# Kernel tuning notes

Measured on AMD Instinct MI355X. Metric: run time of the kernel, lower is better.

Reference implementation:

```python
import jax, jax.numpy as jnp
import numpy as np

N_FEAT = 7          # input_vector_size
M = 3               # memberships per feature (hardcoded 3 in torch module)
FUZZ = M ** N_FEAT  # 2187, cartesian product size
MID = 512
NUM_CLASS = 10
BATCH = 4096

# Precompute cartesian-product index table: itertools.product over rows of u[i]
# (last feature index varies fastest). IDX[k, i] = which of the 3 memberships of
# feature i appears in combination k.
_k = np.arange(FUZZ)
IDX = ((_k[:, None] // (M ** np.arange(N_FEAT - 1, -1, -1))[None, :]) % M).astype(np.int32)  # [FUZZ, N_FEAT]


def setup_inputs() -> dict:
    key = jax.random.key(0)
    ks = jax.random.split(key, 8)
    x = jax.random.normal(ks[0], (BATCH, N_FEAT), dtype=jnp.float32)
    # Parameters (xavier-ish init for weights, ones for b/bais as in torch init)
    c = jax.random.uniform(ks[1], (N_FEAT, M), minval=-1.0, maxval=1.0, dtype=jnp.float32)
    b = jnp.ones((N_FEAT, M), dtype=jnp.float32)
    wei = jax.random.uniform(ks[2], (FUZZ * N_FEAT, FUZZ), minval=-0.01, maxval=0.01, dtype=jnp.float32)
    bais = jnp.ones((1,), dtype=jnp.float32)
    W1 = jax.random.normal(ks[3], (MID, FUZZ), dtype=jnp.float32) * (1.0 / np.sqrt(FUZZ))
    b1 = jnp.zeros((MID,), dtype=jnp.float32)
    W2 = jax.random.normal(ks[4], (FUZZ, MID), dtype=jnp.float32) * (1.0 / np.sqrt(MID))
    b2 = jnp.zeros((FUZZ,), dtype=jnp.float32)
    W3 = jax.random.normal(ks[5], (NUM_CLASS, FUZZ), dtype=jnp.float32) * (1.0 / np.sqrt(FUZZ))
    b3 = jnp.zeros((NUM_CLASS,), dtype=jnp.float32)
    return {"x": x, "c": c, "b": b, "wei": wei, "bais": bais,
            "W1": W1, "b1": b1, "W2": W2, "b2": b2, "W3": W3, "b3": b3}


def reference(x, c, b, wei, bais, W1, b1, W2, b2, W3, b3):
    B = x.shape[0]
    # Gaussian fuzzy memberships: u[b, i, j] = exp(-(x[b,i]-c[i,j])^2 / b[i,j]^2)
    u = jnp.exp(-((x[:, :, None] - c[None]) ** 2) / (b[None] ** 2))  # [B, N_FEAT, M]
    # Cartesian product: dd[bt, k, i] = u[bt, i, IDX[k, i]]  (replaces itertools.product)
    idx = jnp.asarray(IDX)                       # [FUZZ, N_FEAT]
    feat = jnp.arange(N_FEAT)[None, :]           # [1, N_FEAT] broadcasts to [FUZZ, N_FEAT]
    dd = u[:, feat, idx]                         # [B, FUZZ, N_FEAT]
    # Fuzzy rule layer
    a = dd.reshape(B, FUZZ * N_FEAT) @ wei + bais            # [B, FUZZ]
    a_mean = a / jnp.sum(a, axis=1, keepdims=True)
    # Small residual MLP
    h1 = a_mean @ W1.T + b1                                   # [B, MID]
    h2 = h1 @ W2.T + b2                                       # [B, FUZZ]
    h3 = (a_mean + h2) @ W3.T + b3                            # [B, NUM_CLASS]
    out = jax.nn.leaky_relu(h3, negative_slope=0.2)
    # Dropout(0.5) omitted (eval mode / deterministic baseline)
    return out
```

## Files before the change

kernel.cpp:

```cpp
#include <hip/hip_runtime.h>

#define FUZZ 2187
#define NFEAT 7
#define MID 512
#define NCLS 10
#define BATCH 4096
#define SSTR 2192
#define NCH 243
#define PROWS 11
#define PSTR 2188
#define NF4 546

__device__ __forceinline__ void f4add(float4& a, const float4& b) {
    a.x += b.x; a.y += b.y; a.z += b.z; a.w += b.w;
}

__global__ __launch_bounds__(192) void k_reduce_wei(const float* __restrict__ wei,
                                                    float* __restrict__ Spart) {
    int n4 = blockIdx.x * 192 + threadIdx.x;
    if (n4 > NF4) return;
    int by = blockIdx.y;
    const float* base = wei + (size_t)(by * 9) * 7 * FUZZ;
    float* outp = Spart + (size_t)by * PROWS * PSTR;

    if (n4 < NF4) {
        float4 acc[PROWS];
#pragma unroll
        for (int r = 0; r < PROWS; ++r) acc[r] = make_float4(0.f, 0.f, 0.f, 0.f);
#pragma unroll
        for (int kk = 0; kk < 9; ++kk) {
            const float* rp = base + (size_t)kk * 7 * FUZZ + 4 * n4;
            float4 v0 = *(const float4*)(rp);
            float4 v1 = *(const float4*)(rp + (size_t)1 * FUZZ);
            float4 v2 = *(const float4*)(rp + (size_t)2 * FUZZ);
            float4 v3 = *(const float4*)(rp + (size_t)3 * FUZZ);
            float4 v4 = *(const float4*)(rp + (size_t)4 * FUZZ);
            float4 v5 = *(const float4*)(rp + (size_t)5 * FUZZ);
            float4 v6 = *(const float4*)(rp + (size_t)6 * FUZZ);
            f4add(acc[0], v0);
            f4add(acc[1], v1);
            f4add(acc[2], v2);
            f4add(acc[3], v3);
            f4add(acc[4], v4);
            f4add(acc[5 + kk / 3], v5);
            f4add(acc[8 + kk % 3], v6);
        }
#pragma unroll
        for (int r = 0; r < PROWS; ++r)
            *(float4*)(outp + (size_t)r * PSTR + 4 * n4) = acc[r];
    } else {
        float acc[PROWS][3];
#pragma unroll
        for (int r = 0; r < PROWS; ++r)
            for (int c = 0; c < 3; ++c) acc[r][c] = 0.f;
#pragma unroll
        for (int kk = 0; kk < 9; ++kk) {
            const float* rp = base + (size_t)kk * 7 * FUZZ + 2184;
#pragma unroll
            for (int j = 0; j < 7; ++j) {
                int row = (j < 5) ? j : ((j == 5) ? 5 + kk / 3 : 8 + kk % 3);
#pragma unroll
                for (int c = 0; c < 3; ++c)
                    acc[row][c] += rp[(size_t)j * FUZZ + c];
            }
        }
#pragma unroll
        for (int r = 0; r < PROWS; ++r)
            for (int c = 0; c < 3; ++c)
                outp[(size_t)r * PSTR + 2184 + c] = acc[r][c];
    }
}

__global__ __launch_bounds__(192) void k_reduce2(const float* __restrict__ Spart,
                                                 float* __restrict__ S) {
    int n4 = blockIdx.x * 192 + threadIdx.x;
    if (n4 > NF4) return;
    int t = blockIdx.y;
    int j = t / 3, m = t % 3;

    if (n4 < NF4) {
        float4 s = make_float4(0.f, 0.f, 0.f, 0.f);
        if (j < 5) {
            const int place[5] = {81, 27, 9, 3, 1};
            int ops[4];
            int o = 0;
            for (int q = 0; q < 5; ++q)
                if (q != j) ops[o++] = place[q];
            int byb = m * place[j];
            for (int c = 0; c < 81; ++c) {
                int by = byb + (c / 27) * ops[0] + ((c / 9) % 3) * ops[1]
                             + ((c / 3) % 3) * ops[2] + (c % 3) * ops[3];
                f4add(s, *(const float4*)(Spart + ((size_t)by * PROWS + j) * PSTR + 4 * n4));
            }
        } else {
            int row = (j == 5) ? 5 + m : 8 + m;
            for (int by = 0; by < NCH; ++by)
                f4add(s, *(const float4*)(Spart + ((size_t)by * PROWS + row) * PSTR + 4 * n4));
        }
        *(float4*)(S + (size_t)t * SSTR + 4 * n4) = s;
    } else {
        float s0 = 0.f, s1 = 0.f, s2 = 0.f;
        if (j < 5) {
            const int place[5] = {81, 27, 9, 3, 1};
            int ops[4];
            int o = 0;
            for (int q = 0; q < 5; ++q)
                if (q != j) ops[o++] = place[q];
            int byb = m * place[j];
            for (int c = 0; c < 81; ++c) {
                int by = byb + (c / 27) * ops[0] + ((c / 9) % 3) * ops[1]
                             + ((c / 3) % 3) * ops[2] + (c % 3) * ops[3];
                const float* p = Spart + ((size_t)by * PROWS + j) * PSTR + 2184;
                s0 += p[0]; s1 += p[1]; s2 += p[2];
            }
        } else {
            int row = (j == 5) ? 5 + m : 8 + m;
            for (int by = 0; by < NCH; ++by) {
                const float* p = Spart + ((size_t)by * PROWS + row) * PSTR + 2184;
                s0 += p[0]; s1 += p[1]; s2 += p[2];
            }
        }
        S[(size_t)t * SSTR + 2184] = s0;
        S[(size_t)t * SSTR + 2185] = s1;
        S[(size_t)t * SSTR + 2186] = s2;
    }
}

__device__ __forceinline__ float wave_sum(float v) {
#pragma unroll
    for (int off = 32; off > 0; off >>= 1) v += __shfl_down(v, off, 64);
    return v;
}

__global__ __launch_bounds__(256) void k_sw1(const float* __restrict__ S,
                                             const float* __restrict__ W1,
                                             float* __restrict__ SW1,
                                             float* __restrict__ ws1) {
    int i = blockIdx.x;
    int tid = threadIdx.x;
    float acc[21];
    float aw = 0.f;
#pragma unroll
    for (int t = 0; t < 21; ++t) acc[t] = 0.f;
    for (int n = tid; n < FUZZ; n += 256) {
        float w1 = W1[(size_t)i * FUZZ + n];
        aw += w1;
#pragma unroll
        for (int t = 0; t < 21; ++t) acc[t] += S[t * SSTR + n] * w1;
    }
#pragma unroll
    for (int t = 0; t < 21; ++t) acc[t] = wave_sum(acc[t]);
    aw = wave_sum(aw);
    __shared__ float red[4][22];
    int w = tid >> 6, lane = tid & 63;
    if (lane == 0) {
#pragma unroll
        for (int t = 0; t < 21; ++t) red[w][t] = acc[t];
        red[w][21] = aw;
    }
    __syncthreads();
    if (tid < 22) {
        float v = red[0][tid] + red[1][tid] + red[2][tid] + red[3][tid];
        if (tid < 21) SW1[tid * MID + i] = v;
        else          ws1[i] = v;
    }
}

__global__ __launch_bounds__(64) void k_g(const float* __restrict__ SW1,
                                          const float* __restrict__ ws1,
                                          const float* __restrict__ b1,
                                          const float* __restrict__ W2,
                                          float* __restrict__ G,
                                          float* __restrict__ q,
                                          float* __restrict__ p) {
    int n = blockIdx.x;
    int lane = threadIdx.x;
    float acc[21];
    float aq = 0.f, ap = 0.f;
#pragma unroll
    for (int t = 0; t < 21; ++t) acc[t] = 0.f;
    for (int i = lane; i < MID; i += 64) {
        float w2 = W2[(size_t)n * MID + i];
        aq += ws1[i] * w2;
        ap += b1[i] * w2;
#pragma unroll
        for (int t = 0; t < 21; ++t) acc[t] += SW1[t * MID + i] * w2;
    }
#pragma unroll
    for (int t = 0; t < 21; ++t) acc[t] = wave_sum(acc[t]);
    aq = wave_sum(aq);
    ap = wave_sum(ap);
    if (lane == 0) {
#pragma unroll
        for (int t = 0; t < 21; ++t) G[t * SSTR + n] = acc[t];
        q[n] = aq;
        p[n] = ap;
    }
}

__global__ __launch_bounds__(1024) void k_h(const float* __restrict__ S,
                                            const float* __restrict__ G,
                                            const float* __restrict__ q,
                                            const float* __restrict__ p,
                                            const float* __restrict__ b2,
                                            const float* __restrict__ b3,
                                            const float* __restrict__ W3,
                                            float* __restrict__ H,
                                            float* __restrict__ v,
                                            float* __restrict__ w,
                                            float* __restrict__ T) {
    int c = blockIdx.x;
    int tid = threadIdx.x;
    int wv = tid >> 6, lane = tid & 63;
    __shared__ float red[16][24];
    float acc[21];
#pragma unroll
    for (int t = 0; t < 21; ++t) acc[t] = 0.f;
    if (c < NCLS) {
        float av = 0.f, aw = 0.f;
        for (int n = tid; n < FUZZ; n += 1024) {
            float w3 = W3[(size_t)c * FUZZ + n];
            av += (1.0f + q[n]) * w3;
            aw += (p[n] + b2[n]) * w3;
#pragma unroll
            for (int t = 0; t < 21; ++t)
                acc[t] += (S[t * SSTR + n] + G[t * SSTR + n]) * w3;
        }
#pragma unroll
        for (int t = 0; t < 21; ++t) acc[t] = wave_sum(acc[t]);
        av = wave_sum(av);
        aw = wave_sum(aw);
        if (lane == 0) {
#pragma unroll
            for (int t = 0; t < 21; ++t) red[wv][t] = acc[t];
            red[wv][21] = av;
            red[wv][22] = aw;
        }
        __syncthreads();
        if (tid < 23) {
            float s = 0.f;
#pragma unroll
            for (int k = 0; k < 16; ++k) s += red[k][tid];
            if (tid < 21)       H[tid * NCLS + c] = s;
            else if (tid == 21) v[c] = s;
            else                w[c] = s + b3[c];
        }
    } else {
        for (int n = tid; n < FUZZ; n += 1024) {
#pragma unroll
            for (int t = 0; t < 21; ++t) acc[t] += S[t * SSTR + n];
        }
#pragma unroll
        for (int t = 0; t < 21; ++t) acc[t] = wave_sum(acc[t]);
        if (lane == 0) {
#pragma unroll
            for (int t = 0; t < 21; ++t) red[wv][t] = acc[t];
        }
        __syncthreads();
        if (tid < 21) {
            float s = 0.f;
#pragma unroll
            for (int k = 0; k < 16; ++k) s += red[k][tid];
            T[tid] = s;
        }
    }
}

__global__ __launch_bounds__(256) void k_out(const float* __restrict__ x,
                                             const float* __restrict__ cc,
                                             const float* __restrict__ bbv,
                                             const float* __restrict__ bais,
                                             const float* __restrict__ T,
                                             const float* __restrict__ H,
                                             const float* __restrict__ v,
                                             const float* __restrict__ w,
                                             float* __restrict__ out) {
    int b = blockIdx.x * 256 + threadIdx.x;
    if (b >= BATCH) return;
    float xv[NFEAT];
#pragma unroll
    for (int j = 0; j < NFEAT; ++j) xv[j] = x[b * NFEAT + j];
    float u[21];
#pragma unroll
    for (int j = 0; j < NFEAT; ++j) {
#pragma unroll
        for (int m = 0; m < 3; ++m) {
            float d = xv[j] - cc[j * 3 + m];
            float bv = bbv[j * 3 + m];
            u[j * 3 + m] = expf(-(d * d) / (bv * bv));
        }
    }
    float ba = bais[0];
    float r = 2187.0f * ba;
#pragma unroll
    for (int t = 0; t < 21; ++t) r += u[t] * T[t];
    float inv = 1.0f / r;
#pragma unroll
    for (int c = 0; c < NCLS; ++c) {
        float s = 0.f;
#pragma unroll
        for (int t = 0; t < 21; ++t) s += u[t] * H[t * NCLS + c];
        float h = (s + ba * v[c]) * inv + w[c];
        out[b * NCLS + c] = (h >= 0.f) ? h : 0.2f * h;
    }
}

extern "C" void kernel_launch(void* const* d_in, const int* in_sizes, int n_in,
                              void* d_out, int out_size, void* d_ws, size_t ws_size,
                              hipStream_t stream) {
    const float* x    = (const float*)d_in[0];
    const float* c    = (const float*)d_in[1];
    const float* bbv  = (const float*)d_in[2];
    const float* wei  = (const float*)d_in[3];
    const float* bais = (const float*)d_in[4];
    const float* W1   = (const float*)d_in[5];
    const float* b1   = (const float*)d_in[6];
    const float* W2   = (const float*)d_in[7];
    const float* b2   = (const float*)d_in[8];
    const float* W3   = (const float*)d_in[9];
    const float* b3   = (const float*)d_in[10];

    float* ws    = (float*)d_ws;
    float* Spart = ws;
    float* S     = Spart + 5848528;
    float* G     = S + 21 * SSTR;
    float* SW1   = G + 21 * SSTR;
    float* ws1   = SW1 + 21 * MID;
    float* q     = ws1 + MID;
    float* p     = q + SSTR;
    float* T     = p + SSTR;
    float* H     = T + 32;
    float* v     = H + 224;
    float* w     = v + 16;

    k_reduce_wei<<<dim3(3, NCH), 192, 0, stream>>>(wei, Spart);
    k_reduce2<<<dim3(3, 21), 192, 0, stream>>>(Spart, S);
    k_sw1<<<MID, 256, 0, stream>>>(S, W1, SW1, ws1);
    k_g<<<FUZZ, 64, 0, stream>>>(SW1, ws1, b1, W2, G, q, p);
    k_h<<<NCLS + 1, 1024, 0, stream>>>(S, G, q, p, b2, b3, W3, H, v, w, T);
    k_out<<<(BATCH + 255) / 256, 256, 0, stream>>>(x, c, bbv, bais, T, H, v, w,
                                                   (float*)d_out);
}
```

Measured before the change: 305.1 us.

## Split wei reduction across row groups and vectorize reduction kernels with float4

Adds a z grid dimension to the wei reduction so each block sums only two or seven of the eleven partial rows. This triples the number of blocks streaming the large weight matrix, which should raise memory-level parallelism. The k_sw1, k_g and k_h kernels now use float4 loads and per-lane float4 accumulators, with the 3-element tail handled separately. k_h also drops from 1024 to 256 threads per block. The float4 loads on W1 and W3 rows start at offsets that are not 16-byte aligned because the row length is 2187, which relies on the hardware tolerating unaligned vector loads.

```diff
diff --git a/kernel.cpp b/kernel.cpp
--- a/kernel.cpp
+++ b/kernel.cpp
@@ -14,60 +14,85 @@
 __device__ __forceinline__ void f4add(float4& a, const float4& b) {
     a.x += b.x; a.y += b.y; a.z += b.z; a.w += b.w;
 }
+__device__ __forceinline__ void f4fma(float4& a, const float4& x, const float4& y) {
+    a.x += x.x * y.x; a.y += x.y * y.y; a.z += x.z * y.z; a.w += x.w * y.w;
+}
+__device__ __forceinline__ float f4hsum(const float4& a) {
+    return (a.x + a.y) + (a.z + a.w);
+}
 
 __global__ __launch_bounds__(192) void k_reduce_wei(const float* __restrict__ wei,
                                                     float* __restrict__ Spart) {
     int n4 = blockIdx.x * 192 + threadIdx.x;
     if (n4 > NF4) return;
     int by = blockIdx.y;
+    int z = blockIdx.z;
     const float* base = wei + (size_t)(by * 9) * 7 * FUZZ;
     float* outp = Spart + (size_t)by * PROWS * PSTR;
 
     if (n4 < NF4) {
-        float4 acc[PROWS];
-#pragma unroll
-        for (int r = 0; r < PROWS; ++r) acc[r] = make_float4(0.f, 0.f, 0.f, 0.f);
-#pragma unroll
-        for (int kk = 0; kk < 9; ++kk) {
-            const float* rp = base + (size_t)kk * 7 * FUZZ + 4 * n4;
-            float4 v0 = *(const float4*)(rp);
-            float4 v1 = *(const float4*)(rp + (size_t)1 * FUZZ);
-            float4 v2 = *(const float4*)(rp + (size_t)2 * FUZZ);
-            float4 v3 = *(const float4*)(rp + (size_t)3 * FUZZ);
-            float4 v4 = *(const float4*)(rp + (size_t)4 * FUZZ);
-            float4 v5 = *(const float4*)(rp + (size_t)5 * FUZZ);
-            float4 v6 = *(const float4*)(rp + (size_t)6 * FUZZ);
-            f4add(acc[0], v0);
-            f4add(acc[1], v1);
-            f4add(acc[2], v2);
-            f4add(acc[3], v3);
-            f4add(acc[4], v4);
-            f4add(acc[5 + kk / 3], v5);
-            f4add(acc[8 + kk % 3], v6);
-        }
-#pragma unroll
-        for (int r = 0; r < PROWS; ++r)
-            *(float4*)(outp + (size_t)r * PSTR + 4 * n4) = acc[r];
+        if (z < 2) {
+            int j0 = 2 * z;
+            float4 a0 = make_float4(0.f, 0.f, 0.f, 0.f);
+            float4 a1 = make_float4(0.f, 0.f, 0.f, 0.f);
+#pragma unroll
+            for (int kk = 0; kk < 9; ++kk) {
+                const float* rp = base + (size_t)kk * 7 * FUZZ + (size_t)j0 * FUZZ + 4 * n4;
+                f4add(a0, *(const float4*)(rp));
+                f4add(a1, *(const float4*)(rp + FUZZ));
+            }
+            *(float4*)(outp + (size_t)j0 * PSTR + 4 * n4) = a0;
+            *(float4*)(outp + (size_t)(j0 + 1) * PSTR + 4 * n4) = a1;
+        } else {
+            float4 acc[7];
+#pragma unroll
+            for (int r = 0; r < 7; ++r) acc[r] = make_float4(0.f, 0.f, 0.f, 0.f);
+#pragma unroll
+            for (int kk = 0; kk < 9; ++kk) {
+                const float* rp = base + (size_t)kk * 7 * FUZZ + (size_t)4 * FUZZ + 4 * n4;
+                f4add(acc[0], *(const float4*)(rp));
+                f4add(acc[1 + kk / 3], *(const float4*)(rp + FUZZ));
+                f4add(acc[4 + kk % 3], *(const float4*)(rp + 2 * FUZZ));
+            }
+#pragma unroll
+            for (int r = 0; r < 7; ++r)
+                *(float4*)(outp + (size_t)(4 + r) * PSTR + 4 * n4) = acc[r];
+        }
     } else {
-        float acc[PROWS][3];
-#pragma unroll
-        for (int r = 0; r < PROWS; ++r)
-            for (int c = 0; c < 3; ++c) acc[r][c] = 0.f;
-#pragma unroll
-        for (int kk = 0; kk < 9; ++kk) {
-            const float* rp = base + (size_t)kk * 7 * FUZZ + 2184;
-#pragma unroll
-            for (int j = 0; j < 7; ++j) {
-                int row = (j < 5) ? j : ((j == 5) ? 5 + kk / 3 : 8 + kk % 3);
-#pragma unroll
+        if (z < 2) {
+            int j0 = 2 * z;
+            float a0[3] = {0.f, 0.f, 0.f}, a1[3] = {0.f, 0.f, 0.f};
+#pragma unroll
+            for (int kk = 0; kk < 9; ++kk) {
+                const float* rp = base + (size_t)kk * 7 * FUZZ + (size_t)j0 * FUZZ + 2184;
+#pragma unroll
+                for (int c = 0; c < 3; ++c) { a0[c] += rp[c]; a1[c] += rp[FUZZ + c]; }
+            }
+#pragma unroll
+            for (int c = 0; c < 3; ++c) {
+                outp[(size_t)j0 * PSTR + 2184 + c] = a0[c];
+                outp[(size_t)(j0 + 1) * PSTR + 2184 + c] = a1[c];
+            }
+        } else {
+            float acc[7][3];
+#pragma unroll
+            for (int r = 0; r < 7; ++r)
+                for (int c = 0; c < 3; ++c) acc[r][c] = 0.f;
+#pragma unroll
+            for (int kk = 0; kk < 9; ++kk) {
+                const float* rp = base + (size_t)kk * 7 * FUZZ + (size_t)4 * FUZZ + 2184;
+#pragma unroll
+                for (int c = 0; c < 3; ++c) {
+                    acc[0][c] += rp[c];
+                    acc[1 + kk / 3][c] += rp[FUZZ + c];
+                    acc[4 + kk % 3][c] += rp[2 * FUZZ + c];
+                }
+            }
+#pragma unroll
+            for (int r = 0; r < 7; ++r)
                 for (int c = 0; c < 3; ++c)
-                    acc[row][c] += rp[(size_t)j * FUZZ + c];
-            }
-        }
-#pragma unroll
-        for (int r = 0; r < PROWS; ++r)
-            for (int c = 0; c < 3; ++c)
-                outp[(size_t)r * PSTR + 2184 + c] = acc[r][c];
+                    outp[(size_t)(4 + r) * PSTR + 2184 + c] = acc[r][c];
+        }
     }
 }
 
@@ -138,24 +163,34 @@
                                              float* __restrict__ ws1) {
     int i = blockIdx.x;
     int tid = threadIdx.x;
-    float acc[21];
-    float aw = 0.f;
-#pragma unroll
-    for (int t = 0; t < 21; ++t) acc[t] = 0.f;
-    for (int n = tid; n < FUZZ; n += 256) {
-        float w1 = W1[(size_t)i * FUZZ + n];
-        aw += w1;
-#pragma unroll
-        for (int t = 0; t < 21; ++t) acc[t] += S[t * SSTR + n] * w1;
-    }
-#pragma unroll
-    for (int t = 0; t < 21; ++t) acc[t] = wave_sum(acc[t]);
+    float4 acc[21];
+    float4 aw4 = make_float4(0.f, 0.f, 0.f, 0.f);
+#pragma unroll
+    for (int t = 0; t < 21; ++t) acc[t] = make_float4(0.f, 0.f, 0.f, 0.f);
+    for (int g = tid; g < NF4; g += 256) {
+        float4 w1 = *(const float4*)(W1 + (size_t)i * FUZZ + 4 * g);
+        f4add(aw4, w1);
+#pragma unroll
+        for (int t = 0; t < 21; ++t)
+            f4fma(acc[t], *(const float4*)(S + (size_t)t * SSTR + 4 * g), w1);
+    }
+    float accs[21], aw = f4hsum(aw4);
+#pragma unroll
+    for (int t = 0; t < 21; ++t) accs[t] = f4hsum(acc[t]);
+    if (tid < 3) {
+        float w1s = W1[(size_t)i * FUZZ + 2184 + tid];
+        aw += w1s;
+#pragma unroll
+        for (int t = 0; t < 21; ++t) accs[t] += S[(size_t)t * SSTR + 2184 + tid] * w1s;
+    }
+#pragma unroll
+    for (int t = 0; t < 21; ++t) accs[t] = wave_sum(accs[t]);
     aw = wave_sum(aw);
     __shared__ float red[4][22];
     int w = tid >> 6, lane = tid & 63;
     if (lane == 0) {
 #pragma unroll
-        for (int t = 0; t < 21; ++t) red[w][t] = acc[t];
+        for (int t = 0; t < 21; ++t) red[w][t] = accs[t];
         red[w][21] = aw;
     }
     __syncthreads();
@@ -175,92 +210,127 @@
                                           float* __restrict__ p) {
     int n = blockIdx.x;
     int lane = threadIdx.x;
-    float acc[21];
-    float aq = 0.f, ap = 0.f;
-#pragma unroll
-    for (int t = 0; t < 21; ++t) acc[t] = 0.f;
-    for (int i = lane; i < MID; i += 64) {
-        float w2 = W2[(size_t)n * MID + i];
-        aq += ws1[i] * w2;
-        ap += b1[i] * w2;
-#pragma unroll
-        for (int t = 0; t < 21; ++t) acc[t] += SW1[t * MID + i] * w2;
-    }
-#pragma unroll
-    for (int t = 0; t < 21; ++t) acc[t] = wave_sum(acc[t]);
-    aq = wave_sum(aq);
-    ap = wave_sum(ap);
+    float4 acc[21];
+    float4 aq4 = make_float4(0.f, 0.f, 0.f, 0.f);
+    float4 ap4 = make_float4(0.f, 0.f, 0.f, 0.f);
+#pragma unroll
+    for (int t = 0; t < 21; ++t) acc[t] = make_float4(0.f, 0.f, 0.f, 0.f);
+#pragma unroll
+    for (int g = lane; g < MID / 4; g += 64) {
+        float4 w2 = *(const float4*)(W2 + (size_t)n * MID + 4 * g);
+        f4fma(aq4, *(const float4*)(ws1 + 4 * g), w2);
+        f4fma(ap4, *(const float4*)(b1 + 4 * g), w2);
+#pragma unroll
+        for (int t = 0; t < 21; ++t)
+            f4fma(acc[t], *(const float4*)(SW1 + (size_t)t * MID + 4 * g), w2);
+    }
+    float accs[21];
+#pragma unroll
+    for (int t = 0; t < 21; ++t) accs[t] = wave_sum(f4hsum(acc[t]));
+    float aq = wave_sum(f4hsum(aq4));
+    float ap = wave_sum(f4hsum(ap4));
     if (lane == 0) {
 #pragma unroll
-        for (int t = 0; t < 21; ++t) G[t * SSTR + n] = acc[t];
+        for (int t = 0; t < 21; ++t) G[t * SSTR + n] = accs[t];
         q[n] = aq;
         p[n] = ap;
     }
 }
 
-__global__ __launch_bounds__(1024) void k_h(const float* __restrict__ S,
-                                            const float* __restrict__ G,
-                                            const float* __restrict__ q,
-                                            const float* __restrict__ p,
-                                            const float* __restrict__ b2,
-                                            const float* __restrict__ b3,
-                                            const float* __restrict__ W3,
-                                            float* __restrict__ H,
-                                            float* __restrict__ v,
-                                            float* __restrict__ w,
-                                            float* __restrict__ T) {
+__global__ __launch_bounds__(256) void k_h(const float* __restrict__ S,
+                                           const float* __restrict__ G,
+                                           const float* __restrict__ q,
+                                           const float* __restrict__ p,
+                                           const float* __restrict__ b2,
+                                           const float* __restrict__ b3,
+                                           const float* __restrict__ W3,
+                                           float* __restrict__ H,
+                                           float* __restrict__ v,
+                                           float* __restrict__ w,
+                                           float* __restrict__ T) {
     int c = blockIdx.x;
     int tid = threadIdx.x;
     int wv = tid >> 6, lane = tid & 63;
-    __shared__ float red[16][24];
-    float acc[21];
-#pragma unroll
-    for (int t = 0; t < 21; ++t) acc[t] = 0.f;
+    __shared__ float red[4][24];
     if (c < NCLS) {
-        float av = 0.f, aw = 0.f;
-        for (int n = tid; n < FUZZ; n += 1024) {
+        float4 acc[21];
+        float4 av4 = make_float4(0.f, 0.f, 0.f, 0.f);
+        float4 aw4 = make_float4(0.f, 0.f, 0.f, 0.f);
+#pragma unroll
+        for (int t = 0; t < 21; ++t) acc[t] = make_float4(0.f, 0.f, 0.f, 0.f);
+        for (int g = tid; g < NF4; g += 256) {
+            float4 w3 = *(const float4*)(W3 + (size_t)c * FUZZ + 4 * g);
+            float4 qv = *(const float4*)(q + 4 * g);
+            float4 pv = *(const float4*)(p + 4 * g);
+            float4 bv = *(const float4*)(b2 + 4 * g);
+            av4.x += (1.f + qv.x) * w3.x; av4.y += (1.f + qv.y) * w3.y;
+            av4.z += (1.f + qv.z) * w3.z; av4.w += (1.f + qv.w) * w3.w;
+            aw4.x += (pv.x + bv.x) * w3.x; aw4.y += (pv.y + bv.y) * w3.y;
+            aw4.z += (pv.z + bv.z) * w3.z; aw4.w += (pv.w + bv.w) * w3.w;
+#pragma unroll
+            for (int t = 0; t < 21; ++t) {
+                float4 sv = *(const float4*)(S + (size_t)t * SSTR + 4 * g);
+                float4 gv = *(const float4*)(G + (size_t)t * SSTR + 4 * g);
+                acc[t].x += (sv.x + gv.x) * w3.x;
+                acc[t].y += (sv.y + gv.y) * w3.y;
+                acc[t].z += (sv.z + gv.z) * w3.z;
+                acc[t].w += (sv.w + gv.w) * w3.w;
+            }
+        }
+        float accs[21], av = f4hsum(av4), aw = f4hsum(aw4);
+#pragma unroll
+        for (int t = 0; t < 21; ++t) accs[t] = f4hsum(acc[t]);
+        if (tid < 3) {
+            int n = 2184 + tid;
             float w3 = W3[(size_t)c * FUZZ + n];
-            av += (1.0f + q[n]) * w3;
+            av += (1.f + q[n]) * w3;
             aw += (p[n] + b2[n]) * w3;
 #pragma unroll
             for (int t = 0; t < 21; ++t)
-                acc[t] += (S[t * SSTR + n] + G[t * SSTR + n]) * w3;
-        }
-#pragma unroll
-        for (int t = 0; t < 21; ++t) acc[t] = wave_sum(acc[t]);
+                accs[t] += (S[(size_t)t * SSTR + n] + G[(size_t)t * SSTR + n]) * w3;
+        }
+#pragma unroll
+        for (int t = 0; t < 21; ++t) accs[t] = wave_sum(accs[t]);
         av = wave_sum(av);
         aw = wave_sum(aw);
         if (lane == 0) {
 #pragma unroll
-            for (int t = 0; t < 21; ++t) red[wv][t] = acc[t];
+            for (int t = 0; t < 21; ++t) red[wv][t] = accs[t];
             red[wv][21] = av;
             red[wv][22] = aw;
         }
         __syncthreads();
         if (tid < 23) {
-            float s = 0.f;
-#pragma unroll
-            for (int k = 0; k < 16; ++k) s += red[k][tid];
+            float s = red[0][tid] + red[1][tid] + red[2][tid] + red[3][tid];
             if (tid < 21)       H[tid * NCLS + c] = s;
             else if (tid == 21) v[c] = s;
             else                w[c] = s + b3[c];
         }
     } else {
-        for (int n = tid; n < FUZZ; n += 1024) {
-#pragma unroll
-            for (int t = 0; t < 21; ++t) acc[t] += S[t * SSTR + n];
-        }
-#pragma unroll
-        for (int t = 0; t < 21; ++t) acc[t] = wave_sum(acc[t]);
+        float4 acc[21];
+#pragma unroll
+        for (int t = 0; t < 21; ++t) acc[t] = make_float4(0.f, 0.f, 0.f, 0.f);
+        for (int g = tid; g < NF4; g += 256) {
+#pragma unroll
+            for (int t = 0; t < 21; ++t)
+                f4add(acc[t], *(const float4*)(S + (size_t)t * SSTR + 4 * g));
+        }
+        float accs[21];
+#pragma unroll
+        for (int t = 0; t < 21; ++t) accs[t] = f4hsum(acc[t]);
+        if (tid < 3) {
+#pragma unroll
+            for (int t = 0; t < 21; ++t) accs[t] += S[(size_t)t * SSTR + 2184 + tid];
+        }
+#pragma unroll
+        for (int t = 0; t < 21; ++t) accs[t] = wave_sum(accs[t]);
         if (lane == 0) {
 #pragma unroll
-            for (int t = 0; t < 21; ++t) red[wv][t] = acc[t];
+            for (int t = 0; t < 21; ++t) red[wv][t] = accs[t];
         }
         __syncthreads();
         if (tid < 21) {
-            float s = 0.f;
-#pragma unroll
-            for (int k = 0; k < 16; ++k) s += red[k][tid];
+            float s = red[0][tid] + red[1][tid] + red[2][tid] + red[3][tid];
             T[tid] = s;
         }
     }
@@ -333,11 +403,11 @@
     float* v     = H + 224;
     float* w     = v + 16;
 
-    k_reduce_wei<<<dim3(3, NCH), 192, 0, stream>>>(wei, Spart);
+    k_reduce_wei<<<dim3(3, NCH, 3), 192, 0, stream>>>(wei, Spart);
     k_reduce2<<<dim3(3, 21), 192, 0, stream>>>(Spart, S);
     k_sw1<<<MID, 256, 0, stream>>>(S, W1, SW1, ws1);
     k_g<<<FUZZ, 64, 0, stream>>>(SW1, ws1, b1, W2, G, q, p);
-    k_h<<<NCLS + 1, 1024, 0, stream>>>(S, G, q, p, b2, b3, W3, H, v, w, T);
+    k_h<<<NCLS + 1, 256, 0, stream>>>(S, G, q, p, b2, b3, W3, H, v, w, T);
     k_out<<<(BATCH + 255) / 256, 256, 0, stream>>>(x, c, bbv, bais, T, H, v, w,
                                                    (float*)d_out);
 }
```

After: 309.6 us. Within noise of the previous version (+1.5%).
